# Kernel optimization log

Hardware: AMD Instinct MI355X
Metric: run time of the kernel (lower is better)

Reference implementation:

```python
import jax, jax.numpy as jnp
import numpy as np

# Neighbor offsets (di, dj) implied by each 3x3 kernel: out_j = gray - shift(gray, di, dj)
# kernel0..kernel7 as defined in the torch module (center weight +1, one neighbor -1)
OFFSETS = [(0, -1), (1, -1), (1, 0), (1, 1), (0, 1), (-1, 1), (-1, 0), (-1, -1)]
EPS = 1e-5  # torch InstanceNorm2d default


def setup_inputs() -> dict:
    key = jax.random.key(0)
    x = jax.random.uniform(key, (8, 3, 1024, 1024), dtype=jnp.float32)
    return {"x": x}


def _ltpe(x):
    # RGB -> gray, [B,1,H,W]
    g = (0.3 * x[:, 0] + 0.59 * x[:, 1] + 0.11 * x[:, 2])[:, None]
    B, _, H, W = g.shape
    gp = jnp.pad(g, ((0, 0), (0, 0), (1, 1), (1, 1)))  # zero pad = conv padding=1
    out = jnp.zeros_like(g)
    for j, (di, dj) in enumerate(OFFSETS):
        nb = gp[:, :, 1 + di:1 + di + H, 1 + dj:1 + dj + W]
        d = (g - nb + 1.0) * 0.5          # (conv_out + 1) * 0.5
        out = out + d * (float(2 ** j) / 255.0)
    # InstanceNorm2d(1): per (b, c) mean/biased-var over spatial dims, no affine
    mean = jnp.mean(out, axis=(2, 3), keepdims=True)
    var = jnp.var(out, axis=(2, 3), keepdims=True)
    out = (out - mean) * jax.lax.rsqrt(var + EPS)
    return jnp.concatenate([out, out, out], axis=1)  # [B,3,H,W]


def reference(x):
    return _ltpe(x)
```

## Files before the change

kernel.cpp:

```cpp
#include <hip/hip_runtime.h>
#include <hip/hip_cooperative_groups.h>
#include <math.h>

namespace cg = cooperative_groups;

constexpr int H = 1024, W = 1024, B = 8;
constexpr int NPIX = H * W;

constexpr int FR    = 16;
constexpr int GPB   = H / FR;
constexpr int FGRID = B * GPB;

__device__ __forceinline__ void gload16(const float* g, float* l) {
    __builtin_amdgcn_global_load_lds(
        (const __attribute__((address_space(1))) void*)g,
        (__attribute__((address_space(3))) void*)l, 16, 0, 0);
}
__device__ __forceinline__ float grayat(const float* __restrict__ xb, int r, int c) {
    const float* p = xb + (size_t)r * W + c;
    return 0.3f * p[0] + 0.59f * p[NPIX] + 0.11f * p[2 * NPIX];
}

__global__ __launch_bounds__(256, 2)
void ltpe_fused(const float* __restrict__ x, float* __restrict__ out,
                float2* __restrict__ part)
{
    __shared__ float lds[4][5][3][256];
    __shared__ float2 wred[4];

    const int blk  = blockIdx.x;
    const int b    = blk & 7;
    const int g    = blk >> 3;
    const int r0   = g * FR;
    const int tid  = threadIdx.x;
    const int w    = tid >> 6;
    const int lane = tid & 63;
    const int c    = tid << 2;
    const float* xb = x + (size_t)b * 3 * NPIX;
    float (*ldsw)[3][256] = lds[w];

    constexpr float w0 = 1.f/255.f,  w1 = 2.f/255.f,  w2 = 4.f/255.f,  w3 = 8.f/255.f,
                    w4 = 16.f/255.f, w5 = 32.f/255.f, w6 = 64.f/255.f, w7 = 128.f/255.f;

    float pL[FR + 2], pR[FR + 2];
    #pragma unroll
    for (int i = 0; i < FR + 2; ++i) { pL[i] = 0.f; pR[i] = 0.f; }
    if (lane == 0 && c > 0) {
        #pragma unroll
        for (int i = 0; i < FR + 2; ++i) {
            const int rr = r0 - 1 + i;
            if ((unsigned)rr < (unsigned)H) pL[i] = grayat(xb, rr, c - 1);
        }
    }
    if (lane == 63 && c + 4 < W) {
        #pragma unroll
        for (int i = 0; i < FR + 2; ++i) {
            const int rr = r0 - 1 + i;
            if ((unsigned)rr < (unsigned)H) pR[i] = grayat(xb, rr, c + 4);
        }
    }
    __builtin_amdgcn_sched_barrier(0);

    auto stage = [&](int off, int slot) {
        int rr = r0 - 1 + off;
        rr = rr < 0 ? 0 : (rr > H - 1 ? H - 1 : rr);
        const float* gp = xb + (size_t)rr * W + (w << 8) + (lane << 2);
        gload16(gp,            &ldsw[slot][0][0]);
        gload16(gp + NPIX,     &ldsw[slot][1][0]);
        gload16(gp + 2*NPIX,   &ldsw[slot][2][0]);
    };

    auto grayc = [&](int off, int slot, float (&d)[6]) {
        const bool rok = (unsigned)(r0 - 1 + off) < (unsigned)H;
        const float4 a = *reinterpret_cast<const float4*>(&ldsw[slot][0][lane << 2]);
        const float4 e = *reinterpret_cast<const float4*>(&ldsw[slot][1][lane << 2]);
        const float4 f = *reinterpret_cast<const float4*>(&ldsw[slot][2][lane << 2]);
        float g1 = 0.3f*a.x + 0.59f*e.x + 0.11f*f.x;
        float g2 = 0.3f*a.y + 0.59f*e.y + 0.11f*f.y;
        float g3 = 0.3f*a.z + 0.59f*e.z + 0.11f*f.z;
        float g4 = 0.3f*a.w + 0.59f*e.w + 0.11f*f.w;
        float glv = __shfl_up(g4, 1);
        float grv = __shfl_down(g1, 1);
        if (lane == 0)  glv = pL[off];
        if (lane == 63) grv = pR[off];
        if (!rok) { g1 = g2 = g3 = g4 = glv = grv = 0.f; }
        d[0]=glv; d[1]=g1; d[2]=g2; d[3]=g3; d[4]=g4; d[5]=grv;
    };

    float gr6[3][6];
    float4 tq[FR];
    float s = 0.f, ss = 0.f;

    stage(0, 0); stage(1, 1); stage(2, 2); stage(3, 3);
    asm volatile("s_waitcnt vmcnt(6)" ::: "memory");
    __builtin_amdgcn_sched_barrier(0);
    grayc(0, 0, gr6[0]);
    grayc(1, 1, gr6[1]);

#define LTPE_STEP(I, WAITSTR)                                                  \
    {                                                                          \
        if ((I) + 4 <= FR + 1) stage((I) + 4, ((I) + 4) % 5);                  \
        asm volatile(WAITSTR ::: "memory");                                    \
        __builtin_amdgcn_sched_barrier(0);                                     \
        grayc((I) + 2, ((I) + 2) % 5, gr6[((I) + 2) % 3]);                     \
        const float (&up)[6] = gr6[(I) % 3];                                   \
        const float (&mi)[6] = gr6[((I) + 1) % 3];                             \
        const float (&dn)[6] = gr6[((I) + 2) % 3];                             \
        float tv[4];                                                           \
        _Pragma("unroll")                                                      \
        for (int kk = 0; kk < 4; ++kk) {                                       \
            float sv = w0 * mi[kk];                                            \
            sv = fmaf(w1, dn[kk],     sv);                                     \
            sv = fmaf(w2, dn[kk + 1], sv);                                     \
            sv = fmaf(w3, dn[kk + 2], sv);                                     \
            sv = fmaf(w4, mi[kk + 2], sv);                                     \
            sv = fmaf(w5, up[kk + 2], sv);                                     \
            sv = fmaf(w6, up[kk + 1], sv);                                     \
            sv = fmaf(w7, up[kk],     sv);                                     \
            tv[kk] = 0.5f * mi[kk + 1] + 0.5f - 0.5f * sv;                     \
            s += tv[kk];                                                       \
            ss = fmaf(tv[kk], tv[kk], ss);                                     \
        }                                                                      \
        tq[I] = make_float4(tv[0], tv[1], tv[2], tv[3]);                       \
    }

    LTPE_STEP(0,  "s_waitcnt vmcnt(6)")
    LTPE_STEP(1,  "s_waitcnt vmcnt(6)")
    LTPE_STEP(2,  "s_waitcnt vmcnt(6)")
    LTPE_STEP(3,  "s_waitcnt vmcnt(6)")
    LTPE_STEP(4,  "s_waitcnt vmcnt(6)")
    LTPE_STEP(5,  "s_waitcnt vmcnt(6)")
    LTPE_STEP(6,  "s_waitcnt vmcnt(6)")
    LTPE_STEP(7,  "s_waitcnt vmcnt(6)")
    LTPE_STEP(8,  "s_waitcnt vmcnt(6)")
    LTPE_STEP(9,  "s_waitcnt vmcnt(6)")
    LTPE_STEP(10, "s_waitcnt vmcnt(6)")
    LTPE_STEP(11, "s_waitcnt vmcnt(6)")
    LTPE_STEP(12, "s_waitcnt vmcnt(6)")
    LTPE_STEP(13, "s_waitcnt vmcnt(6)")
    LTPE_STEP(14, "s_waitcnt vmcnt(3)")
    LTPE_STEP(15, "s_waitcnt vmcnt(0)")
#undef LTPE_STEP

    #pragma unroll
    for (int off = 32; off >= 1; off >>= 1) {
        s  += __shfl_down(s, off);
        ss += __shfl_down(ss, off);
    }
    if (lane == 0) wred[w] = make_float2(s, ss);
    __syncthreads();
    if (tid == 0) {
        float2 a0 = wred[0], a1 = wred[1], a2 = wred[2], a3 = wred[3];
        part[(size_t)b * GPB + g] = make_float2(a0.x + a1.x + a2.x + a3.x,
                                                a0.y + a1.y + a2.y + a3.y);
    }

    cg::this_grid().sync();

    const float2 pv = part[(size_t)b * GPB + lane];
    double ds = (double)pv.x, dss = (double)pv.y;
    #pragma unroll
    for (int o = 1; o <= 32; o <<= 1) {
        ds  += __shfl_xor(ds, o);
        dss += __shfl_xor(dss, o);
    }
    const double n     = (double)NPIX;
    const double dmean = ds / n;
    const double dvar  = dss / n - dmean * dmean;
    const float mean = (float)dmean;
    const float rstd = (float)(1.0 / sqrt(dvar + 1e-5));

    float* ob = out + (size_t)b * 3 * NPIX + (size_t)r0 * W + c;
    #pragma unroll
    for (int i = 0; i < FR; ++i) {
        const float4 t4 = tq[i];
        float4 y;
        y.x = (t4.x - mean) * rstd;
        y.y = (t4.y - mean) * rstd;
        y.z = (t4.z - mean) * rstd;
        y.w = (t4.w - mean) * rstd;
        float* p = ob + (size_t)i * W;
        *reinterpret_cast<float4*>(p)            = y;
        *reinterpret_cast<float4*>(p + NPIX)     = y;
        *reinterpret_cast<float4*>(p + 2 * NPIX) = y;
    }
}

constexpr int ROWS = 2;
constexpr int RG   = H / ROWS;

__global__ __launch_bounds__(256)
void ltpe_stage1(const float* __restrict__ x, float* __restrict__ out,
                 float2* __restrict__ part)
{
    __shared__ float lds[4][3][W];
    const int b   = blockIdx.y;
    const int k   = blockIdx.x;
    const int kg  = ((k & 7) << 6) | (k >> 3);
    const int r0  = kg * ROWS;
    const int tid = threadIdx.x;
    const int w   = tid >> 6;
    const int l   = tid & 63;
    const int c   = tid << 2;
    const float* xb = x + (size_t)b * 3 * NPIX;

    #pragma unroll
    for (int s = 0; s < 4; ++s) {
        const int rr = r0 - 1 + s;
        if ((unsigned)rr < (unsigned)H) {
            #pragma unroll
            for (int ch = 0; ch < 3; ++ch) {
                const float* gp = xb + (size_t)ch * NPIX + (size_t)rr * W + (w << 8) + (l << 2);
                gload16(gp, &lds[s][ch][w << 8]);
            }
        } else {
            const float4 z = make_float4(0.f, 0.f, 0.f, 0.f);
            #pragma unroll
            for (int ch = 0; ch < 3; ++ch)
                *reinterpret_cast<float4*>(&lds[s][ch][c]) = z;
        }
    }
    __syncthreads();

    const int ql = (tid == 0)   ? 0   : tid - 1;
    const int qr = (tid == 255) ? 255 : tid + 1;
    float g6[4][6];
    #pragma unroll
    for (int s = 0; s < 4; ++s) {
        const float4 o0 = *reinterpret_cast<const float4*>(&lds[s][0][c]);
        const float4 o1 = *reinterpret_cast<const float4*>(&lds[s][1][c]);
        const float4 o2 = *reinterpret_cast<const float4*>(&lds[s][2][c]);
        const float4 l0 = *reinterpret_cast<const float4*>(&lds[s][0][ql << 2]);
        const float4 l1 = *reinterpret_cast<const float4*>(&lds[s][1][ql << 2]);
        const float4 l2 = *reinterpret_cast<const float4*>(&lds[s][2][ql << 2]);
        const float4 rq0 = *reinterpret_cast<const float4*>(&lds[s][0][qr << 2]);
        const float4 rq1 = *reinterpret_cast<const float4*>(&lds[s][1][qr << 2]);
        const float4 rq2 = *reinterpret_cast<const float4*>(&lds[s][2][qr << 2]);
        g6[s][1] = 0.3f * o0.x + 0.59f * o1.x + 0.11f * o2.x;
        g6[s][2] = 0.3f * o0.y + 0.59f * o1.y + 0.11f * o2.y;
        g6[s][3] = 0.3f * o0.z + 0.59f * o1.z + 0.11f * o2.z;
        g6[s][4] = 0.3f * o0.w + 0.59f * o1.w + 0.11f * o2.w;
        g6[s][0] = (tid == 0)   ? 0.f : 0.3f * l0.w  + 0.59f * l1.w  + 0.11f * l2.w;
        g6[s][5] = (tid == 255) ? 0.f : 0.3f * rq0.x + 0.59f * rq1.x + 0.11f * rq2.x;
    }

    constexpr float w0 = 1.f/255.f,  w1 = 2.f/255.f,  w2 = 4.f/255.f,  w3 = 8.f/255.f,
                    w4 = 16.f/255.f, w5 = 32.f/255.f, w6 = 64.f/255.f, w7 = 128.f/255.f;
    float s = 0.f, ss = 0.f;
    float* ob = out + (size_t)b * 3 * NPIX + (size_t)r0 * W + c;
    #pragma unroll
    for (int rr = 0; rr < ROWS; ++rr) {
        const float (&up)[6] = g6[rr];
        const float (&mi)[6] = g6[rr + 1];
        const float (&dn)[6] = g6[rr + 2];
        float tv[4];
        #pragma unroll
        for (int kk = 0; kk < 4; ++kk) {
            float sv = w0 * mi[kk];
            sv = fmaf(w1, dn[kk],     sv);
            sv = fmaf(w2, dn[kk + 1], sv);
            sv = fmaf(w3, dn[kk + 2], sv);
            sv = fmaf(w4, mi[kk + 2], sv);
            sv = fmaf(w5, up[kk + 2], sv);
            sv = fmaf(w6, up[kk + 1], sv);
            sv = fmaf(w7, up[kk],     sv);
            tv[kk] = 0.5f * mi[kk + 1] + 0.5f - 0.5f * sv;
            s += tv[kk];
            ss = fmaf(tv[kk], tv[kk], ss);
        }
        float4 t4 = {tv[0], tv[1], tv[2], tv[3]};
        *reinterpret_cast<float4*>(ob + (size_t)rr * W) = t4;
    }

    #pragma unroll
    for (int off = 32; off >= 1; off >>= 1) {
        s  += __shfl_down(s, off);
        ss += __shfl_down(ss, off);
    }
    __shared__ float2 wred[4];
    if (l == 0) wred[w] = make_float2(s, ss);
    __syncthreads();
    if (tid == 0) {
        float2 a0 = wred[0], a1 = wred[1], a2 = wred[2], a3 = wred[3];
        part[(size_t)b * RG + kg] = make_float2(a0.x + a1.x + a2.x + a3.x,
                                                a0.y + a1.y + a2.y + a3.y);
    }
}

__global__ __launch_bounds__(256)
void ltpe_stageB(float* __restrict__ out, const float2* __restrict__ part)
{
    const int b    = blockIdx.y;
    const int r    = blockIdx.x;
    const int tid  = threadIdx.x;
    const int lane = tid & 63;

    const float4* pp = reinterpret_cast<const float4*>(part + (size_t)b * RG);
    const float4 u = pp[tid];
    double s  = (double)u.x + (double)u.z;
    double ss = (double)u.y + (double)u.w;
    #pragma unroll
    for (int off = 32; off >= 1; off >>= 1) {
        s  += __shfl_down(s, off);
        ss += __shfl_down(ss, off);
    }
    __shared__ double red[8];
    __shared__ float2 mv;
    const int wv = tid >> 6;
    if (lane == 0) { red[wv] = s; red[4 + wv] = ss; }
    __syncthreads();
    if (tid == 0) {
        const double S  = red[0] + red[1] + red[2] + red[3];
        const double SS = red[4] + red[5] + red[6] + red[7];
        const double n    = (double)NPIX;
        const double mean = S / n;
        const double var  = SS / n - mean * mean;
        mv = make_float2((float)mean, (float)(1.0 / sqrt(var + 1e-5)));
    }
    __syncthreads();
    const float mean = mv.x, rstd = mv.y;

    const size_t base = (size_t)b * 3 * NPIX + (size_t)r * W + (tid << 2);
    const float4 t4 = *reinterpret_cast<const float4*>(out + base);
    float4 y;
    y.x = (t4.x - mean) * rstd;
    y.y = (t4.y - mean) * rstd;
    y.z = (t4.z - mean) * rstd;
    y.w = (t4.w - mean) * rstd;
    *reinterpret_cast<float4*>(out + base)            = y;
    *reinterpret_cast<float4*>(out + base + NPIX)     = y;
    *reinterpret_cast<float4*>(out + base + 2 * NPIX) = y;
}

extern "C" void kernel_launch(void* const* d_in, const int* in_sizes, int n_in,
                              void* d_out, int out_size, void* d_ws, size_t ws_size,
                              hipStream_t stream)
{
    const float* x = (const float*)d_in[0];
    float* out = (float*)d_out;
    float2* part = (float2*)d_ws;

    int nb = 0;
    hipError_t qe = hipOccupancyMaxActiveBlocksPerMultiprocessor(
        &nb, reinterpret_cast<const void*>(ltpe_fused), 256, 0);

    if (qe == hipSuccess && nb * 256 >= FGRID) {
        void* args[] = { (void*)&x, (void*)&out, (void*)&part };
        hipLaunchCooperativeKernel((void*)ltpe_fused, dim3(FGRID), dim3(256),
                                   args, 0, stream);
    } else {
        ltpe_stage1<<<dim3(RG, B), 256, 0, stream>>>(x, out, part);
        ltpe_stageB<<<dim3(H, B), 256, 0, stream>>>(out, part);
    }
}
```

Before: 50.89 us.

## Replace grid sync with per-batch atomic counters, deepen prefetch, use nontemporal stores

Drops the cooperative-groups grid barrier and has each block publish its partial sums with atomics and spin on a per-batch counter, so a batch proceeds once its 64 blocks have arrived instead of waiting on the whole grid. The LDS prefetch pipeline is deepened from four rows to five in flight, with the wait counts adjusted. Output stores become nontemporal to avoid polluting the cache. This adds a memset launch for the counters, spin-wait traffic on those counters, and relies on all blocks of a batch being co-resident.

```diff
diff --git a/kernel.cpp b/kernel.cpp
--- a/kernel.cpp
+++ b/kernel.cpp
@@ -1,11 +1,10 @@
 #include <hip/hip_runtime.h>
-#include <hip/hip_cooperative_groups.h>
 #include <math.h>
-
-namespace cg = cooperative_groups;
 
 constexpr int H = 1024, W = 1024, B = 8;
 constexpr int NPIX = H * W;
+
+typedef float f32x4 __attribute__((ext_vector_type(4)));
 
 constexpr int FR    = 16;
 constexpr int GPB   = H / FR;
@@ -20,10 +19,16 @@
     const float* p = xb + (size_t)r * W + c;
     return 0.3f * p[0] + 0.59f * p[NPIX] + 0.11f * p[2 * NPIX];
 }
+__device__ __forceinline__ void nt_store4(float* p, float x, float y, float z, float w) {
+    f32x4 v = {x, y, z, w};
+    __builtin_nontemporal_store(v, reinterpret_cast<f32x4*>(p));
+}
+
+union PackF2 { float2 f; unsigned long long u; };
 
 __global__ __launch_bounds__(256, 2)
 void ltpe_fused(const float* __restrict__ x, float* __restrict__ out,
-                float2* __restrict__ part)
+                float2* __restrict__ part, unsigned* __restrict__ cnt)
 {
     __shared__ float lds[4][5][3][256];
     __shared__ float2 wred[4];
@@ -59,6 +64,7 @@
             if ((unsigned)rr < (unsigned)H) pR[i] = grayat(xb, rr, c + 4);
         }
     }
+    asm volatile("s_waitcnt vmcnt(0)" ::: "memory");
     __builtin_amdgcn_sched_barrier(0);
 
     auto stage = [&](int off, int slot) {
@@ -91,15 +97,15 @@
     float4 tq[FR];
     float s = 0.f, ss = 0.f;
 
-    stage(0, 0); stage(1, 1); stage(2, 2); stage(3, 3);
-    asm volatile("s_waitcnt vmcnt(6)" ::: "memory");
+    stage(0, 0); stage(1, 1); stage(2, 2); stage(3, 3); stage(4, 4);
+    asm volatile("s_waitcnt vmcnt(9)" ::: "memory");
     __builtin_amdgcn_sched_barrier(0);
     grayc(0, 0, gr6[0]);
     grayc(1, 1, gr6[1]);
 
 #define LTPE_STEP(I, WAITSTR)                                                  \
     {                                                                          \
-        if ((I) + 4 <= FR + 1) stage((I) + 4, ((I) + 4) % 5);                  \
+        if ((I) + 5 <= FR + 1) stage((I) + 5, ((I) + 5) % 5);                  \
         asm volatile(WAITSTR ::: "memory");                                    \
         __builtin_amdgcn_sched_barrier(0);                                     \
         grayc((I) + 2, ((I) + 2) % 5, gr6[((I) + 2) % 3]);                     \
@@ -124,19 +130,19 @@
         tq[I] = make_float4(tv[0], tv[1], tv[2], tv[3]);                       \
     }
 
-    LTPE_STEP(0,  "s_waitcnt vmcnt(6)")
-    LTPE_STEP(1,  "s_waitcnt vmcnt(6)")
-    LTPE_STEP(2,  "s_waitcnt vmcnt(6)")
-    LTPE_STEP(3,  "s_waitcnt vmcnt(6)")
-    LTPE_STEP(4,  "s_waitcnt vmcnt(6)")
-    LTPE_STEP(5,  "s_waitcnt vmcnt(6)")
-    LTPE_STEP(6,  "s_waitcnt vmcnt(6)")
-    LTPE_STEP(7,  "s_waitcnt vmcnt(6)")
-    LTPE_STEP(8,  "s_waitcnt vmcnt(6)")
-    LTPE_STEP(9,  "s_waitcnt vmcnt(6)")
-    LTPE_STEP(10, "s_waitcnt vmcnt(6)")
-    LTPE_STEP(11, "s_waitcnt vmcnt(6)")
-    LTPE_STEP(12, "s_waitcnt vmcnt(6)")
+    LTPE_STEP(0,  "s_waitcnt vmcnt(9)")
+    LTPE_STEP(1,  "s_waitcnt vmcnt(9)")
+    LTPE_STEP(2,  "s_waitcnt vmcnt(9)")
+    LTPE_STEP(3,  "s_waitcnt vmcnt(9)")
+    LTPE_STEP(4,  "s_waitcnt vmcnt(9)")
+    LTPE_STEP(5,  "s_waitcnt vmcnt(9)")
+    LTPE_STEP(6,  "s_waitcnt vmcnt(9)")
+    LTPE_STEP(7,  "s_waitcnt vmcnt(9)")
+    LTPE_STEP(8,  "s_waitcnt vmcnt(9)")
+    LTPE_STEP(9,  "s_waitcnt vmcnt(9)")
+    LTPE_STEP(10, "s_waitcnt vmcnt(9)")
+    LTPE_STEP(11, "s_waitcnt vmcnt(9)")
+    LTPE_STEP(12, "s_waitcnt vmcnt(9)")
     LTPE_STEP(13, "s_waitcnt vmcnt(6)")
     LTPE_STEP(14, "s_waitcnt vmcnt(3)")
     LTPE_STEP(15, "s_waitcnt vmcnt(0)")
@@ -149,16 +155,29 @@
     }
     if (lane == 0) wred[w] = make_float2(s, ss);
     __syncthreads();
+
     if (tid == 0) {
         float2 a0 = wred[0], a1 = wred[1], a2 = wred[2], a3 = wred[3];
-        part[(size_t)b * GPB + g] = make_float2(a0.x + a1.x + a2.x + a3.x,
-                                                a0.y + a1.y + a2.y + a3.y);
-    }
-
-    cg::this_grid().sync();
-
-    const float2 pv = part[(size_t)b * GPB + lane];
-    double ds = (double)pv.x, dss = (double)pv.y;
+        PackF2 pk;
+        pk.f = make_float2(a0.x + a1.x + a2.x + a3.x,
+                           a0.y + a1.y + a2.y + a3.y);
+        __hip_atomic_store(
+            reinterpret_cast<unsigned long long*>(&part[(size_t)b * GPB + g]),
+            pk.u, __ATOMIC_RELAXED, __HIP_MEMORY_SCOPE_AGENT);
+        __hip_atomic_fetch_add(&cnt[b], 1u, __ATOMIC_RELEASE,
+                               __HIP_MEMORY_SCOPE_AGENT);
+        while (__hip_atomic_load(&cnt[b], __ATOMIC_ACQUIRE,
+                                 __HIP_MEMORY_SCOPE_AGENT) < (unsigned)GPB) {
+            __builtin_amdgcn_s_sleep(1);
+        }
+    }
+    __syncthreads();
+
+    PackF2 pv;
+    pv.u = __hip_atomic_load(
+        reinterpret_cast<const unsigned long long*>(&part[(size_t)b * GPB + lane]),
+        __ATOMIC_RELAXED, __HIP_MEMORY_SCOPE_AGENT);
+    double ds = (double)pv.f.x, dss = (double)pv.f.y;
     #pragma unroll
     for (int o = 1; o <= 32; o <<= 1) {
         ds  += __shfl_xor(ds, o);
@@ -174,15 +193,14 @@
     #pragma unroll
     for (int i = 0; i < FR; ++i) {
         const float4 t4 = tq[i];
-        float4 y;
-        y.x = (t4.x - mean) * rstd;
-        y.y = (t4.y - mean) * rstd;
-        y.z = (t4.z - mean) * rstd;
-        y.w = (t4.w - mean) * rstd;
+        const float yx = (t4.x - mean) * rstd;
+        const float yy = (t4.y - mean) * rstd;
+        const float yz = (t4.z - mean) * rstd;
+        const float yw = (t4.w - mean) * rstd;
         float* p = ob + (size_t)i * W;
-        *reinterpret_cast<float4*>(p)            = y;
-        *reinterpret_cast<float4*>(p + NPIX)     = y;
-        *reinterpret_cast<float4*>(p + 2 * NPIX) = y;
+        nt_store4(p,            yx, yy, yz, yw);
+        nt_store4(p + NPIX,     yx, yy, yz, yw);
+        nt_store4(p + 2 * NPIX, yx, yy, yz, yw);
     }
 }
 
@@ -339,15 +357,17 @@
     const float* x = (const float*)d_in[0];
     float* out = (float*)d_out;
     float2* part = (float2*)d_ws;
+    unsigned* cnt = (unsigned*)((char*)d_ws + 32768);
 
     int nb = 0;
     hipError_t qe = hipOccupancyMaxActiveBlocksPerMultiprocessor(
         &nb, reinterpret_cast<const void*>(ltpe_fused), 256, 0);
 
     if (qe == hipSuccess && nb * 256 >= FGRID) {
-        void* args[] = { (void*)&x, (void*)&out, (void*)&part };
-        hipLaunchCooperativeKernel((void*)ltpe_fused, dim3(FGRID), dim3(256),
-                                   args, 0, stream);
+        (void)hipMemsetAsync(cnt, 0, 8 * sizeof(unsigned), stream);
+        void* args[] = { (void*)&x, (void*)&out, (void*)&part, (void*)&cnt };
+        (void)hipLaunchCooperativeKernel((void*)ltpe_fused, dim3(FGRID), dim3(256),
+                                         args, 0, stream);
     } else {
         ltpe_stage1<<<dim3(RG, B), 256, 0, stream>>>(x, out, part);
         ltpe_stageB<<<dim3(H, B), 256, 0, stream>>>(out, part);
```

Measured after the change: 50.98 us. No clear change (+0.2%).
